# Kernel tuning notes

Measured on AMD Instinct MI355X. Metric: run time of the kernel, lower is better.

## Reference

```python
import jax, jax.numpy as jnp
import numpy as np

E, D_IN, D_OUT, A, R, T = 8, 1024, 1024, 4, 16, 8192


def setup_inputs() -> dict:
    key = jax.random.key(0)
    ks = jax.random.split(key, 6)
    x = jax.random.normal(ks[0], (T, D_IN), jnp.float32)
    weight = jax.random.normal(ks[1], (E, D_IN, D_OUT), jnp.float32) / np.float32(np.sqrt(D_IN))
    # he_uniform-like scale for lora_A; lora_B random (zeros in real init would hide the LoRA path)
    lora_A = jax.random.normal(ks[2], (A, E, D_IN, R), jnp.float32) * np.float32(np.sqrt(2.0 / D_IN))
    lora_B = jax.random.normal(ks[3], (A, E, R, D_OUT), jnp.float32) * np.float32(0.02)
    lora_scaling = jax.random.uniform(ks[4], (A,), jnp.float32, 0.5, 1.5)
    group_sizes = jnp.full((E,), T // E, dtype=jnp.int32)  # sums to T
    adapter_indices_sorted = jax.random.randint(ks[5], (T,), 0, A, dtype=jnp.int32)
    return {
        'x': x, 'weight': weight, 'lora_A': lora_A, 'lora_B': lora_B,
        'lora_scaling': lora_scaling, 'group_sizes': group_sizes,
        'adapter_indices_sorted': adapter_indices_sorted,
    }


def reference(x, weight, lora_A, lora_B, lora_scaling, group_sizes, adapter_indices_sorted):
    total_tokens, d_in = x.shape
    n_experts, _, d_out = weight.shape
    n_adapters, _, _, rank = lora_A.shape
    n_groups = n_adapters * n_experts

    # Base expert-grouped GEMM: x is already sorted by expert via group_sizes.
    base_out = jax.lax.ragged_dot(x, weight, group_sizes)  # [T, d_out]

    # Combined (adapter, expert) group id per token.
    expert_idx = jnp.repeat(jnp.arange(n_experts), group_sizes, total_repeat_length=total_tokens)
    flat_idx = adapter_indices_sorted * n_experts + expert_idx  # [T]

    # prepare_routing: stable sort tokens by combined group id.
    sort_idx = jnp.argsort(flat_idx, stable=True)
    x_sorted = x[sort_idx]
    combined_group_sizes = jnp.zeros((n_groups,), jnp.int32).at[flat_idx].add(1)
    unsort_idx = jnp.argsort(sort_idx)

    # Nested LoRA grouped GEMMs over flattened (adapter, expert) groups.
    lora_A_flat = lora_A.reshape(n_groups, d_in, rank)
    lora_B_flat = lora_B.reshape(n_groups, rank, d_out)
    intermediate = jax.lax.ragged_dot(x_sorted, lora_A_flat, combined_group_sizes)  # [T, rank]
    lora_out_sorted = jax.lax.ragged_dot(intermediate, lora_B_flat, combined_group_sizes)  # [T, d_out]

    lora_out = lora_out_sorted[unsort_idx] * lora_scaling[adapter_indices_sorted, None]
    return base_out + lora_out
```

## Files before the change

### kernel.cpp

```cpp
#include <hip/hip_runtime.h>
#include <hip/hip_bf16.h>
#include <stdint.h>


#define T_TOK 8192
#define DIN   1024
#define DOUT  1024
#define NE    8
#define NA    4
#define RK    16
#define KEXT  1088
#define NOCT  136

typedef __attribute__((ext_vector_type(8))) short short8;
typedef __attribute__((ext_vector_type(4))) float f32x4;

__device__ __forceinline__ ushort f2bf(float f) {
  union { float f; uint32_t i; } v; v.f = f;
  uint32_t x = v.i;
  return (ushort)((x + 0x7fffu + ((x >> 16) & 1u)) >> 16);
}

__device__ __forceinline__ void gload_lds16(const void* g, void* l) {
  __builtin_amdgcn_global_load_lds(
      (const __attribute__((address_space(1))) uint32_t*)g,
      (__attribute__((address_space(3))) uint32_t*)l,
      16, 0, 0);
}

__device__ __forceinline__ int expert_of_row(const int* __restrict__ gs, int row) {
  int cum = 0, e = 0;
#pragma unroll
  for (int i = 0; i < NE; ++i) { if (row >= cum) e = i; cum += gs[i]; }
  return e;
}

__global__ __launch_bounds__(256) void k_prepA(
    const float* __restrict__ lora_A, const float* __restrict__ lora_scaling,
    ushort* __restrict__ Aoct) {
  const int bid = blockIdx.x;
  const int tid = threadIdx.x;
  int u = bid * 4 + (tid >> 6);
  int e = u >> 7, ko = u & 127;
  int c = tid & 63;
  int a = c >> 4, r = c & 15;
  float s = lora_scaling[a];
  ushort o8[8];
#pragma unroll
  for (int j = 0; j < 8; ++j) {
    float v = lora_A[((size_t)(a * NE + e) * DIN + ko * 8 + j) * RK + r];
    o8[j] = f2bf(s * v);
  }
  *(uint4*)(Aoct + ((size_t)((e * 128 + ko) * 64 + c)) * 8) = *(const uint4*)o8;
}

__global__ __launch_bounds__(256) void k_main(
    const float* __restrict__ x, ushort* __restrict__ xp,
    const ushort* __restrict__ Aoct,
    const float* __restrict__ weight, const float* __restrict__ lora_B,
    ushort* __restrict__ Boct,
    const int* __restrict__ gs, const int* __restrict__ adapter_idx) {
  __shared__ ushort As2[16 * 64];
  __shared__ ushort Bs2[8 * 64 * 8];

  const int bid = blockIdx.x;
  const int tid = threadIdx.x;

  if (bid < 512) {
    const int lane = tid & 63;
    const int wave = tid >> 6;
    const int rows0 = bid * 16;
    const int e = expert_of_row(gs, rows0);
    const ushort* aoct = Aoct + (size_t)e * 128 * 64 * 8;

    const int row = tid >> 4;
    const int seg = tid & 15;
    const int r7 = row & 7;

    f32x4 acc = (f32x4){0.f, 0.f, 0.f, 0.f};

    for (int kt = 0; kt < 16; ++kt) {
#pragma unroll
      for (int rd = 0; rd < 2; ++rd) {
        int o = wave * 2 + rd;
        const ushort* src = aoct + ((size_t)(kt * 8 + o) * 64 + lane) * 8;
        gload_lds16(src, &Bs2[o * 64 * 8]);
      }

      const float* srcx = x + (size_t)(rows0 + row) * DIN + kt * 64 + seg * 4;
      float4 q = *(const float4*)srcx;
      ushort4 b;
      b.x = f2bf(q.x); b.y = f2bf(q.y); b.z = f2bf(q.z); b.w = f2bf(q.w);
      *(ushort4*)(xp + (size_t)(rows0 + row) * KEXT + kt * 64 + seg * 4) = b;
      int ch = (seg >> 1) ^ r7;
      *(ushort4*)&As2[row * 64 + ch * 8 + (seg & 1) * 4] = b;

      __syncthreads();

      int m = lane & 15;
#pragma unroll
      for (int h = 0; h < 2; ++h) {
        int kblk = h * 4 + (lane >> 4);
        short8 af = *(const short8*)&As2[m * 64 + (kblk ^ (m & 7)) * 8];
        short8 bfv = *(const short8*)&Bs2[(kblk * 64 + wave * 16 + m) * 8];
        acc = __builtin_amdgcn_mfma_f32_16x16x32_bf16(af, bfv, acc, 0, 0, 0);
      }
      __syncthreads();
    }

#pragma unroll
    for (int i = 0; i < 4; ++i) {
      int grow = rows0 + (lane >> 4) * 4 + i;
      int a_row = adapter_idx[grow];
      float val = (a_row == wave) ? acc[i] : 0.f;
      xp[(size_t)grow * KEXT + DIN + wave * 16 + (lane & 15)] = f2bf(val);
    }
  } else {
    int e, ko;
    const float* srcbase = nullptr;
    if (bid < 1536) {
      int u = bid - 512;
      e = u >> 7; ko = u & 127;
      srcbase = weight + (size_t)e * DIN * DOUT + (size_t)(ko * 8) * DOUT;
    } else {
      int u = bid - 1536;
      e = u >> 3; int o = u & 7; ko = 128 + o;
    }
    int n4 = tid * 4;
    float v[8][4];
    if (bid < 1536) {
#pragma unroll
      for (int j = 0; j < 8; ++j) {
        float4 q = *(const float4*)(srcbase + (size_t)j * DOUT + n4);
        v[j][0] = q.x; v[j][1] = q.y; v[j][2] = q.z; v[j][3] = q.w;
      }
    } else {
      int o = ko - 128;
#pragma unroll
      for (int j = 0; j < 8; ++j) {
        int kv = o * 8 + j;
        int a = kv >> 4, r = kv & 15;
        float4 q = *(const float4*)(lora_B + (size_t)((a * NE + e) * RK + r) * DOUT + n4);
        v[j][0] = q.x; v[j][1] = q.y; v[j][2] = q.z; v[j][3] = q.w;
      }
    }
    ushort* dst = Boct + ((size_t)(e * NOCT + ko) * DOUT + n4) * 8;
#pragma unroll
    for (int i = 0; i < 4; ++i) {
      ushort o8[8];
#pragma unroll
      for (int j = 0; j < 8; ++j) o8[j] = f2bf(v[j][i]);
      *(uint4*)(dst + i * 8) = *(const uint4*)o8;
    }
  }
}

__global__ __launch_bounds__(256) void k_gemm(
    const ushort* __restrict__ xp, const ushort* __restrict__ Boct,
    const int* __restrict__ gs, float* __restrict__ out) {
  __shared__ ushort As[128 * 64];
  __shared__ ushort Bs[8 * 128 * 8];

  const int tid = threadIdx.x;
  const int lane = tid & 63;
  const int wave = tid >> 6;
  const int wm = wave >> 1, wn = wave & 1;

  const int bid = blockIdx.x;
  const int swz = (bid & 7) * 64 + (bid >> 3);
  const int row0 = (swz >> 3) * 128;
  const int n0 = (swz & 7) * 128;
  const int e = expert_of_row(gs, row0);
  const ushort* boct = Boct + (size_t)e * NOCT * DOUT * 8;

  f32x4 acc[4][4];
#pragma unroll
  for (int mi = 0; mi < 4; ++mi)
#pragma unroll
    for (int ni = 0; ni < 4; ++ni) acc[mi][ni] = (f32x4){0.f, 0.f, 0.f, 0.f};

  const int r8 = lane >> 3;
  const int c8s = (lane & 7) ^ r8;

  for (int kt = 0; kt < 17; ++kt) {
#pragma unroll
    for (int rd = 0; rd < 4; ++rd) {
      int r = wave * 32 + rd * 8 + r8;
      const ushort* src = xp + (size_t)(row0 + r) * KEXT + kt * 64 + c8s * 8;
      gload_lds16(src, &As[(wave * 32 + rd * 8) * 64]);
    }
#pragma unroll
    for (int rd = 0; rd < 4; ++rd) {
      int u = wave * 4 + rd;
      int o = u >> 1, hf = u & 1;
      const ushort* src = boct + ((size_t)(kt * 8 + o) * DOUT + n0 + hf * 64 + lane) * 8;
      gload_lds16(src, &Bs[(o * 128 + hf * 64) * 8]);
    }
    __syncthreads();

#pragma unroll
    for (int h = 0; h < 2; ++h) {
      int kblk = h * 4 + (lane >> 4);
      short8 af[4], bfv[4];
#pragma unroll
      for (int mi = 0; mi < 4; ++mi) {
        int m = wm * 64 + mi * 16 + (lane & 15);
        af[mi] = *(const short8*)&As[m * 64 + (kblk ^ (m & 7)) * 8];
      }
#pragma unroll
      for (int ni = 0; ni < 4; ++ni) {
        int n = wn * 64 + ni * 16 + (lane & 15);
        bfv[ni] = *(const short8*)&Bs[(kblk * 128 + n) * 8];
      }
#pragma unroll
      for (int mi = 0; mi < 4; ++mi)
#pragma unroll
        for (int ni = 0; ni < 4; ++ni)
          acc[mi][ni] = __builtin_amdgcn_mfma_f32_16x16x32_bf16(
              af[mi], bfv[ni], acc[mi][ni], 0, 0, 0);
    }
    __syncthreads();
  }

#pragma unroll
  for (int mi = 0; mi < 4; ++mi) {
#pragma unroll
    for (int ni = 0; ni < 4; ++ni) {
      int col = n0 + wn * 64 + ni * 16 + (lane & 15);
#pragma unroll
      for (int i = 0; i < 4; ++i) {
        int r = row0 + wm * 64 + mi * 16 + (lane >> 4) * 4 + i;
        out[(size_t)r * DOUT + col] = acc[mi][ni][i];
      }
    }
  }
}

extern "C" void kernel_launch(void* const* d_in, const int* in_sizes, int n_in,
                              void* d_out, int out_size, void* d_ws, size_t ws_size,
                              hipStream_t stream) {
  const float* x            = (const float*)d_in[0];
  const float* weight       = (const float*)d_in[1];
  const float* lora_A       = (const float*)d_in[2];
  const float* lora_B       = (const float*)d_in[3];
  const float* lora_scaling = (const float*)d_in[4];
  const int*   group_sizes  = (const int*)d_in[5];
  const int*   adapter_idx  = (const int*)d_in[6];
  float* out = (float*)d_out;

  const size_t sz_xp    = (size_t)T_TOK * KEXT * 2;
  const size_t sz_boct  = (size_t)NE * NOCT * DOUT * 8 * 2;
  ushort* xp   = (ushort*)d_ws;
  ushort* boct = (ushort*)((char*)d_ws + sz_xp);
  ushort* aoct = (ushort*)((char*)d_ws + sz_xp + sz_boct);

  k_prepA<<<256, 256, 0, stream>>>(lora_A, lora_scaling, aoct);
  k_main<<<1600, 256, 0, stream>>>(x, xp, aoct, weight, lora_B, boct,
                                   group_sizes, adapter_idx);
  k_gemm<<<512, 256, 0, stream>>>(xp, boct, group_sizes, out);
}
```

Measured before the change: 159.2 us.

## Fold LoRA-A prep into main kernel and split x conversion into separate blocks

Removes the separate k_prepA launch. The LoRA-A intermediate blocks now read fp32 x and lora_A directly into MFMA registers, converting and scaling on the fly with no LDS staging or barriers. The x-to-bf16 conversion into xp moves to 1024 new dedicated blocks, and LoRA-A blocks are interleaved across experts by a swizzled block index. This saves one launch and the barrier-bound staging, but each wave does strided scalar loads of lora_A (stride RK), reloads x rows per wave, and x is now read twice.

```diff
diff --git a/kernel.cpp b/kernel.cpp
--- a/kernel.cpp
+++ b/kernel.cpp
@@ -35,100 +35,82 @@
   return e;
 }
 
-__global__ __launch_bounds__(256) void k_prepA(
-    const float* __restrict__ lora_A, const float* __restrict__ lora_scaling,
-    ushort* __restrict__ Aoct) {
-  const int bid = blockIdx.x;
-  const int tid = threadIdx.x;
-  int u = bid * 4 + (tid >> 6);
-  int e = u >> 7, ko = u & 127;
-  int c = tid & 63;
-  int a = c >> 4, r = c & 15;
-  float s = lora_scaling[a];
-  ushort o8[8];
-#pragma unroll
-  for (int j = 0; j < 8; ++j) {
-    float v = lora_A[((size_t)(a * NE + e) * DIN + ko * 8 + j) * RK + r];
-    o8[j] = f2bf(s * v);
-  }
-  *(uint4*)(Aoct + ((size_t)((e * 128 + ko) * 64 + c)) * 8) = *(const uint4*)o8;
-}
-
 __global__ __launch_bounds__(256) void k_main(
     const float* __restrict__ x, ushort* __restrict__ xp,
-    const ushort* __restrict__ Aoct,
+    const float* __restrict__ lora_A, const float* __restrict__ lora_scaling,
     const float* __restrict__ weight, const float* __restrict__ lora_B,
     ushort* __restrict__ Boct,
     const int* __restrict__ gs, const int* __restrict__ adapter_idx) {
-  __shared__ ushort As2[16 * 64];
-  __shared__ ushort Bs2[8 * 64 * 8];
-
   const int bid = blockIdx.x;
   const int tid = threadIdx.x;
 
   if (bid < 512) {
+    const int vb = (bid & 7) * 64 + (bid >> 3);
     const int lane = tid & 63;
     const int wave = tid >> 6;
-    const int rows0 = bid * 16;
+    const int rows0 = vb * 16;
     const int e = expert_of_row(gs, rows0);
-    const ushort* aoct = Aoct + (size_t)e * 128 * 64 * 8;
-
-    const int row = tid >> 4;
-    const int seg = tid & 15;
-    const int r7 = row & 7;
+    const int m = lane & 15;
+    const int kg = lane >> 4;
+    const float s = lora_scaling[wave];
+    const float* la = lora_A + (size_t)(wave * NE + e) * DIN * RK + m;
+    const float* xr = x + (size_t)(rows0 + m) * DIN;
 
     f32x4 acc = (f32x4){0.f, 0.f, 0.f, 0.f};
 
     for (int kt = 0; kt < 16; ++kt) {
 #pragma unroll
-      for (int rd = 0; rd < 2; ++rd) {
-        int o = wave * 2 + rd;
-        const ushort* src = aoct + ((size_t)(kt * 8 + o) * 64 + lane) * 8;
-        gload_lds16(src, &Bs2[o * 64 * 8]);
-      }
-
-      const float* srcx = x + (size_t)(rows0 + row) * DIN + kt * 64 + seg * 4;
-      float4 q = *(const float4*)srcx;
-      ushort4 b;
-      b.x = f2bf(q.x); b.y = f2bf(q.y); b.z = f2bf(q.z); b.w = f2bf(q.w);
-      *(ushort4*)(xp + (size_t)(rows0 + row) * KEXT + kt * 64 + seg * 4) = b;
-      int ch = (seg >> 1) ^ r7;
-      *(ushort4*)&As2[row * 64 + ch * 8 + (seg & 1) * 4] = b;
-
-      __syncthreads();
-
-      int m = lane & 15;
-#pragma unroll
       for (int h = 0; h < 2; ++h) {
-        int kblk = h * 4 + (lane >> 4);
-        short8 af = *(const short8*)&As2[m * 64 + (kblk ^ (m & 7)) * 8];
-        short8 bfv = *(const short8*)&Bs2[(kblk * 64 + wave * 16 + m) * 8];
-        acc = __builtin_amdgcn_mfma_f32_16x16x32_bf16(af, bfv, acc, 0, 0, 0);
-      }
-      __syncthreads();
+        const int kblk = h * 4 + kg;
+        const int k0 = kt * 64 + kblk * 8;
+        float4 a0 = *(const float4*)(xr + k0);
+        float4 a1 = *(const float4*)(xr + k0 + 4);
+        short8 af;
+        af[0] = (short)f2bf(a0.x); af[1] = (short)f2bf(a0.y);
+        af[2] = (short)f2bf(a0.z); af[3] = (short)f2bf(a0.w);
+        af[4] = (short)f2bf(a1.x); af[5] = (short)f2bf(a1.y);
+        af[6] = (short)f2bf(a1.z); af[7] = (short)f2bf(a1.w);
+        short8 bf;
+#pragma unroll
+        for (int j = 0; j < 8; ++j)
+          bf[j] = (short)f2bf(s * la[(size_t)(k0 + j) * RK]);
+        acc = __builtin_amdgcn_mfma_f32_16x16x32_bf16(af, bf, acc, 0, 0, 0);
+      }
     }
 
 #pragma unroll
     for (int i = 0; i < 4; ++i) {
-      int grow = rows0 + (lane >> 4) * 4 + i;
+      int grow = rows0 + kg * 4 + i;
       int a_row = adapter_idx[grow];
       float val = (a_row == wave) ? acc[i] : 0.f;
-      xp[(size_t)grow * KEXT + DIN + wave * 16 + (lane & 15)] = f2bf(val);
+      xp[(size_t)grow * KEXT + DIN + wave * 16 + m] = f2bf(val);
+    }
+  } else if (bid < 1536) {
+    int idx = (bid - 512) * 2048 + tid * 8;
+#pragma unroll
+    for (int i = 0; i < 8; ++i) {
+      int u = idx + i;
+      int row = u >> 8;
+      int c4 = u & 255;
+      float4 v = *(const float4*)(x + (size_t)row * DIN + c4 * 4);
+      ushort4 b;
+      b.x = f2bf(v.x); b.y = f2bf(v.y); b.z = f2bf(v.z); b.w = f2bf(v.w);
+      *(ushort4*)(xp + (size_t)row * KEXT + c4 * 4) = b;
     }
   } else {
     int e, ko;
     const float* srcbase = nullptr;
-    if (bid < 1536) {
-      int u = bid - 512;
+    if (bid < 2560) {
+      int u = bid - 1536;
       e = u >> 7; ko = u & 127;
       srcbase = weight + (size_t)e * DIN * DOUT + (size_t)(ko * 8) * DOUT;
     } else {
-      int u = bid - 1536;
+      int u = bid - 2560;
       e = u >> 3; int o = u & 7; ko = 128 + o;
     }
     int n4 = tid * 4;
     float v[8][4];
-    if (bid < 1536) {
+    if (bid < 2560) {
 #pragma unroll
       for (int j = 0; j < 8; ++j) {
         float4 q = *(const float4*)(srcbase + (size_t)j * DOUT + n4);
@@ -248,14 +230,12 @@
   const int*   adapter_idx  = (const int*)d_in[6];
   float* out = (float*)d_out;
 
-  const size_t sz_xp    = (size_t)T_TOK * KEXT * 2;
-  const size_t sz_boct  = (size_t)NE * NOCT * DOUT * 8 * 2;
+  const size_t sz_xp = (size_t)T_TOK * KEXT * 2;
   ushort* xp   = (ushort*)d_ws;
   ushort* boct = (ushort*)((char*)d_ws + sz_xp);
-  ushort* aoct = (ushort*)((char*)d_ws + sz_xp + sz_boct);
-
-  k_prepA<<<256, 256, 0, stream>>>(lora_A, lora_scaling, aoct);
-  k_main<<<1600, 256, 0, stream>>>(x, xp, aoct, weight, lora_B, boct,
+
+  k_main<<<2624, 256, 0, stream>>>(x, xp, lora_A, lora_scaling,
+                                   weight, lora_B, boct,
                                    group_sizes, adapter_idx);
   k_gemm<<<512, 256, 0, stream>>>(xp, boct, group_sizes, out);
 }
```

After: 167.0 us. +4.9%, slower.
